# Optimization experiments

Measured on AMD Instinct MI355X. Metric: run time of the kernel, lower is better.

Reference implementation:

```python
import jax, jax.numpy as jnp
import numpy as np

N, C, T, V = 64, 64, 128, 25
OUT, REL = 64, 8
MID = OUT // 2
BN_EPS = 1e-5


def _conv1x1(x, w, b):
    # 1x1 Conv2d: x [n,c,h,w_], w [o,c], b [o]
    return jnp.einsum('nchw,oc->nohw', x, w) + b[None, :, None, None]


def _forward(x, A, w1, b1, w2, b2, w11, b11, w22, b22, w3, b3, w4, b4,
             watt, batt, w5, b5, wc1, bc1, bn_g, bn_b, bn_m, bn_v,
             wc2, bc2, ws, bs, beita, alpha):
    T_ = x.shape[2]
    rel = w1.shape[0]
    x1 = _conv1x1(x, w1, b1)                          # [N,rel,T,V]
    x2 = _conv1x1(x, w2, b2)
    x1_mean, x2_mean = x1.mean(2), x2.mean(2)         # [N,rel,V]
    x1_max, x2_max = x1.max(2), x2.max(2)
    mean_res = x1_mean[:, :, :, None] - x2_mean[:, :, None, :]   # [N,rel,V,V]
    max_res = x1_max[:, :, :, None] - x2_max[:, :, None, :]
    # conv5: grouped 1x1 conv (groups=rel, 2 in-ch/group). The cat(dim=2)+reshape
    # interleaves channels as (mean[c], max[c]) pairs, so per-group it is:
    x_1 = jnp.tanh(w5[None, :, 0, None, None] * mean_res
                   + w5[None, :, 1, None, None] * max_res
                   + b5[None, :, None, None]) * alpha
    x_1 = _conv1x1(x_1, w4, b4)                       # [N,out,V,V]
    x3 = _conv1x1(x, w3, b3)                          # [N,out,T,V]
    x1_res = x_1 + A[None, None]
    # channel-wise spatial correlation attention
    att = jnp.tanh(jnp.einsum('nctu,nctv->ncuv', x1, x2) / T_)
    att = _conv1x1(att, watt, batt)                   # [N,out,V,V]
    global_res = jnp.einsum('nctu,ncuv->nctv', x3, att)
    # Bi_Inter 'channel': global avg pool -> 1x1 -> BN(inference) -> GELU -> 1x1 -> sigmoid
    g = global_res.mean((2, 3), keepdims=True)        # [N,out,1,1]
    h = _conv1x1(g, wc1, bc1)
    h = (h - bn_m[None, :, None, None]) * (bn_g[None, :, None, None]
        / jnp.sqrt(bn_v[None, :, None, None] + BN_EPS)) + bn_b[None, :, None, None]
    h = jax.nn.gelu(h, approximate=False)
    c_att = jax.nn.sigmoid(_conv1x1(h, wc2, bc2))     # [N,out,1,1]
    x1_res = c_att * x1_res
    x1_res = jnp.einsum('ncuv,nctv->nctu', x1_res, x3)  # [N,out,T,V]
    # Bi_Inter 'spatial': mean over T -> 1x1 (out->1) -> sigmoid
    s_att = jax.nn.sigmoid(_conv1x1(x1_res.mean(2, keepdims=True), ws, bs))  # [N,1,1,V]
    global_res = global_res * s_att
    x1_res = x1_res + global_res
    # per-frame spatial correlation (temporal branch)
    x11 = _conv1x1(x, w11, b11)
    x22 = _conv1x1(x, w22, b22)
    xt = jnp.tanh(jnp.einsum('nctv,nctu->ntvu', x11, x22) / rel)  # [N,T,V,V]
    t_res = jnp.einsum('nctu,ntuv->nctv', x3, xt)
    return t_res * beita + x1_res                     # [N,out,T,V]


def setup_inputs() -> dict:
    key = jax.random.key(0)
    ks = jax.random.split(key, 16)
    def nrm(i, shape, s=0.05):
        return jax.random.normal(ks[i], shape, jnp.float32) * s
    return {
        'x': jax.random.normal(ks[0], (N, C, T, V), jnp.float32),
        'A': nrm(1, (V, V), 0.1),
        'w1': nrm(2, (REL, C)), 'b1': jnp.zeros((REL,), jnp.float32),
        'w2': nrm(3, (REL, C)), 'b2': jnp.zeros((REL,), jnp.float32),
        'w11': nrm(4, (REL, C)), 'b11': jnp.zeros((REL,), jnp.float32),
        'w22': nrm(5, (REL, C)), 'b22': jnp.zeros((REL,), jnp.float32),
        'w3': nrm(6, (OUT, C)), 'b3': jnp.zeros((OUT,), jnp.float32),
        'w4': nrm(7, (OUT, REL)), 'b4': jnp.zeros((OUT,), jnp.float32),
        'watt': nrm(8, (OUT, REL)), 'batt': jnp.zeros((OUT,), jnp.float32),
        'w5': nrm(9, (REL, 2)), 'b5': jnp.zeros((REL,), jnp.float32),
        'wc1': nrm(10, (MID, OUT)), 'bc1': jnp.zeros((MID,), jnp.float32),
        'bn_g': jnp.ones((MID,), jnp.float32), 'bn_b': jnp.zeros((MID,), jnp.float32),
        'bn_m': jnp.zeros((MID,), jnp.float32), 'bn_v': jnp.ones((MID,), jnp.float32),
        'wc2': nrm(11, (OUT, MID)), 'bc2': jnp.zeros((OUT,), jnp.float32),
        'ws': nrm(12, (1, OUT)), 'bs': jnp.zeros((1,), jnp.float32),
        'beita': jnp.full((1,), 0.5, jnp.float32),
        'alpha': 1,
    }


def reference(x, A, w1, b1, w2, b2, w11, b11, w22, b22, w3, b3, w4, b4,
              watt, batt, w5, b5, wc1, bc1, bn_g, bn_b, bn_m, bn_v,
              wc2, bc2, ws, bs, beita, alpha):
    return _forward(x, A, w1, b1, w2, b2, w11, b11, w22, b22, w3, b3, w4, b4,
                    watt, batt, w5, b5, wc1, bc1, bn_g, bn_b, bn_m, bn_v,
                    wc2, bc2, ws, bs, beita, alpha)
```

## Files before the change

kernel.cpp:

```cpp
#include <hip/hip_runtime.h>
#include <hip/hip_bf16.h>
#include <math.h>

#define N_   64
#define C_   64
#define T_   128
#define V_   25
#define OUT_ 64
#define REL_ 8
#define MID_ 32
#define TV_  (T_*V_)
#define VV_  (V_*V_)
#define TT2  8

typedef __hip_bfloat16 bf16;
typedef unsigned int uint;
typedef __attribute__((ext_vector_type(8))) short short8v;
typedef __attribute__((ext_vector_type(4))) float float4v;
__device__ __forceinline__ float b2f(bf16 x){ return __bfloat162float(x); }
__device__ __forceinline__ bf16  f2b(float x){ return __float2bfloat16(x); }
__device__ __forceinline__ float bfu(uint u){ return __uint_as_float(u<<16); }
__device__ __forceinline__ float bfh(uint u){ return __uint_as_float(u&0xffff0000u); }
__device__ __forceinline__ float bfs(unsigned short s){ return __uint_as_float(((uint)s)<<16); }

__device__ __forceinline__ float ftanh(float x){
    float cx = fminf(fmaxf(x, -15.f), 15.f);
    float e  = __expf(2.0f*cx);
    return (e - 1.0f) / (e + 1.0f);
}


__global__ __launch_bounds__(256) void k0_prep(
    const float* __restrict__ w1, const float* __restrict__ b1,
    const float* __restrict__ w2, const float* __restrict__ b2,
    const float* __restrict__ w11, const float* __restrict__ b11,
    const float* __restrict__ w22, const float* __restrict__ b22,
    const float* __restrict__ w3, const float* __restrict__ b3,
    unsigned short* __restrict__ WfragUS, float* __restrict__ Bg)
{
    int tid = threadIdx.x;
    for (int idx = tid; idx < 6144; idx += 256){
        int e  = idx & 7;
        int ln = (idx >> 3) & 63;
        int kb = (idx >> 9) & 1;
        int mt = idx >> 10;
        int m = mt*16 + (ln & 15);
        int k = kb*32 + ((ln >> 4) * 8) + e;
        float w;
        if      (m < 8)  w = w1[m*C_+k];
        else if (m < 16) w = w2[(m-8)*C_+k];
        else if (m < 24) w = w11[(m-16)*C_+k];
        else if (m < 32) w = w22[(m-24)*C_+k];
        else             w = w3[(m-32)*C_+k];
        bf16 h = f2b(w);
        WfragUS[idx] = *(unsigned short*)&h;
    }
    if (tid < 96){
        int o = tid; float bb;
        if      (o < 8)  bb = b1[o];
        else if (o < 16) bb = b2[o-8];
        else if (o < 24) bb = b11[o-16];
        else if (o < 32) bb = b22[o-24];
        else             bb = b3[o-32];
        Bg[o] = bb;
    }
}

__global__ __launch_bounds__(256) void k1_mfma(
    const float* __restrict__ x,
    const unsigned short* __restrict__ WfragUS, const float* __restrict__ Bg,
    bf16* __restrict__ x1h, bf16* __restrict__ x2h,
    bf16* __restrict__ x11h, bf16* __restrict__ x22h,
    bf16* __restrict__ x3h)
{
    __shared__ __align__(16) float xl[C_*64];
    __shared__ float Bl[96];
    int bid = blockIdx.x;
    int n = bid / 50, jt = bid % 50;
    int j0 = jt * 64;
    int tid = threadIdx.x;
    for (int e = tid; e < 1024; e += 256){
        int c = e >> 4, j4 = e & 15;
        ((float4*)xl)[e] = ((const float4*)(x + (size_t)(n*C_+c)*TV_ + j0))[j4];
    }
    if (tid < 96) Bl[tid] = Bg[tid];
    __syncthreads();

    int wave = tid >> 6, lane = tid & 63;
    int l15 = lane & 15, lg = lane >> 4;
    const short8v* wf = (const short8v*)WfragUS;
    short8v a[6][2];
    #pragma unroll
    for (int mt = 0; mt < 6; ++mt)
        #pragma unroll
        for (int kb = 0; kb < 2; ++kb)
            a[mt][kb] = wf[(mt*2 + kb)*64 + lane];
    int jw = wave*16 + l15;
    short8v b[2];
    #pragma unroll
    for (int kb = 0; kb < 2; ++kb){
        short8v bb;
        #pragma unroll
        for (int e = 0; e < 8; ++e){
            bf16 h = f2b(xl[(kb*32 + lg*8 + e)*64 + jw]);
            bb[e] = *(short*)&h;
        }
        b[kb] = bb;
    }
    float4v acc[6];
    #pragma unroll
    for (int mt = 0; mt < 6; ++mt) acc[mt] = (float4v){0.f,0.f,0.f,0.f};
    #pragma unroll
    for (int kb = 0; kb < 2; ++kb)
        #pragma unroll
        for (int mt = 0; mt < 6; ++mt)
            acc[mt] = __builtin_amdgcn_mfma_f32_16x16x32_bf16(a[mt][kb], b[kb], acc[mt], 0, 0, 0);

    int pos = j0 + jw;
    #pragma unroll
    for (int mt = 0; mt < 6; ++mt){
        #pragma unroll
        for (int reg = 0; reg < 4; ++reg){
            int o = mt*16 + lg*4 + reg;
            float val = acc[mt][reg] + Bl[o];
            bf16* dst = (o < 8)  ? x1h  + ((size_t)(n*REL_ + o     ))*TV_
                      : (o < 16) ? x2h  + ((size_t)(n*REL_ + o - 8 ))*TV_
                      : (o < 24) ? x11h + ((size_t)(n*REL_ + o - 16))*TV_
                      : (o < 32) ? x22h + ((size_t)(n*REL_ + o - 24))*TV_
                                 : x3h  + ((size_t)(n*OUT_ + o - 32))*TV_;
            dst[pos] = f2b(val);
        }
    }
}

__global__ __launch_bounds__(256) void k_x3bar2(const bf16* __restrict__ x3h,
                                                float* __restrict__ x3bar)
{
    __shared__ __align__(16) float xf[TV_];
    __shared__ float red[V_*8];
    int bid = blockIdx.x;
    int tid = threadIdx.x;
    for (int e = tid; e < 400; e += 256){
        uint4 p = ((const uint4*)(x3h + (size_t)bid*TV_))[e];
        float* d = xf + e*8;
        d[0]=bfu(p.x); d[1]=bfh(p.x); d[2]=bfu(p.y); d[3]=bfh(p.y);
        d[4]=bfu(p.z); d[5]=bfh(p.z); d[6]=bfu(p.w); d[7]=bfh(p.w);
    }
    __syncthreads();
    if (tid < 200){
        int v = tid % V_, g = tid / V_;
        float s = 0.f;
        #pragma unroll
        for (int k=0;k<16;++k) s += xf[(g*16+k)*V_ + v];
        red[g*V_+v] = s;
    }
    __syncthreads();
    if (tid < V_){
        float s = 0.f;
        #pragma unroll
        for (int g=0; g<8; ++g) s += red[g*V_+tid];
        x3bar[(size_t)bid*V_+tid] = s * (1.0f/T_);
    }
}

__global__ __launch_bounds__(256) void k3_mfma(
    const bf16* __restrict__ x1h, const bf16* __restrict__ x2h,
    const float* __restrict__ w5, const float* __restrict__ b5,
    const int* __restrict__ alpha,
    float* __restrict__ att8T, float* __restrict__ xm)
{
    __shared__ __align__(16) unsigned short l1[TV_], l2[TV_];
    __shared__ float mu1l[V_], mu2l[V_], m1l[V_], m2l[V_];
    int bid = blockIdx.x;
    int tid = threadIdx.x;
    int r = bid % REL_;
    for (int e = tid; e < 400; e += 256){
        ((uint4*)l1)[e] = ((const uint4*)(x1h + (size_t)bid*TV_))[e];
        ((uint4*)l2)[e] = ((const uint4*)(x2h + (size_t)bid*TV_))[e];
    }
    __syncthreads();
    if (tid < 50){
        int v = tid % V_;
        const unsigned short* L = (tid < V_) ? l1 : l2;
        float s=0.f, mm=-1e30f;
        for (int t=0;t<T_;++t){
            float a = bfs(L[t*V_+v]);
            s += a; mm = fmaxf(mm, a);
        }
        if (tid < V_){ mu1l[v]=s*(1.0f/T_); m1l[v]=mm; }
        else         { mu2l[v]=s*(1.0f/T_); m2l[v]=mm; }
    }
    __syncthreads();
    int wave = tid >> 6, lane = tid & 63;
    int l15 = lane & 15, lg = lane >> 4;
    int mt = wave >> 1, nt = wave & 1;
    int mu = mt*16 + l15;
    int nv = nt*16 + l15;
    float4v acc = (float4v){0.f,0.f,0.f,0.f};
    #pragma unroll
    for (int kb = 0; kb < 4; ++kb){
        short8v av, bv;
        #pragma unroll
        for (int e = 0; e < 8; ++e){
            int k = kb*32 + lg*8 + e;
            av[e] = (mu < V_) ? (short)l1[k*V_ + mu] : (short)0;
            bv[e] = (nv < V_) ? (short)l2[k*V_ + nv] : (short)0;
        }
        acc = __builtin_amdgcn_mfma_f32_16x16x32_bf16(av, bv, acc, 0, 0, 0);
    }
    #pragma unroll
    for (int reg = 0; reg < 4; ++reg){
        int u = mt*16 + lg*4 + reg;
        if (u < V_ && nv < V_)
            att8T[(size_t)bid*VV_ + nv*V_ + u] = ftanh(acc[reg]*(1.0f/T_));
    }
    float w50=w5[r*2+0], w51=w5[r*2+1], b5r=b5[r];
    float af = (float)alpha[0];
    for (int idx=tid; idx<VV_; idx+=256){
        int u = idx/V_, v = idx%V_;
        float mr = mu1l[u]-mu2l[v];
        float xr = m1l[u]-m2l[v];
        xm[(size_t)bid*VV_+idx] = ftanh(fmaf(w50,mr,fmaf(w51,xr,b5r))) * af;
    }
}

__global__ __launch_bounds__(256) void k68_catt_satt(
    const float* __restrict__ att8T, const float* __restrict__ xm,
    const float* __restrict__ A, const float* __restrict__ x3bar,
    const float* __restrict__ watt, const float* __restrict__ batt,
    const float* __restrict__ wc1, const float* __restrict__ bc1,
    const float* __restrict__ bng, const float* __restrict__ bnb,
    const float* __restrict__ bnm, const float* __restrict__ bnv,
    const float* __restrict__ wc2, const float* __restrict__ bc2,
    const float* __restrict__ w4, const float* __restrict__ b4,
    const float* __restrict__ wsp, const float* __restrict__ bsp,
    float* __restrict__ catt, float* __restrict__ satt)
{
    __shared__ __align__(16) float xml[REL_*VV_];
    __shared__ __align__(16) float xbl[OUT_*V_];
    __shared__ float Al[VV_];
    __shared__ float w4l[OUT_*REL_];
    __shared__ float rs8[REL_*V_];
    __shared__ float gl[OUT_];
    __shared__ float hl[MID_];
    __shared__ float cattl[OUT_];
    __shared__ float scl[OUT_];
    __shared__ float Wl[REL_*V_];
    __shared__ float Yl[V_];
    __shared__ float red[OUT_];
    int n = blockIdx.x, tid = threadIdx.x;
    for (int e=tid; e<1250; e+=256)
        ((float4*)xml)[e] = ((const float4*)(xm + (size_t)n*REL_*VV_))[e];
    for (int e=tid; e<400; e+=256)
        ((float4*)xbl)[e] = ((const float4*)(x3bar + (size_t)n*OUT_*V_))[e];
    for (int e=tid; e<VV_; e+=256) Al[e] = A[e];
    for (int e=tid; e<OUT_*REL_; e+=256) w4l[e] = w4[e];
    if (tid < REL_*V_){
        int r = tid / V_, u = tid % V_;
        const float* p = att8T + (size_t)(n*REL_+r)*VV_;
        float s = 0.f;
        #pragma unroll
        for (int v=0;v<V_;++v) s += p[v*V_ + u];
        rs8[tid] = s;
    }
    __syncthreads();
    if (tid < OUT_){
        int c = tid;
        const float* xb = xbl + c*V_;
        float xbr[V_], sb = 0.f;
        #pragma unroll
        for (int u=0;u<V_;++u){ xbr[u]=xb[u]; sb += xbr[u]; }
        float s = 0.f;
        #pragma unroll
        for (int r=0;r<REL_;++r){
            float d = 0.f;
            #pragma unroll
            for (int u=0;u<V_;++u) d = fmaf(xbr[u], rs8[r*V_+u], d);
            s = fmaf(watt[c*REL_+r], d, s);
        }
        gl[c] = (s + (float)V_*batt[c]*sb) * (1.0f/(float)V_);
    }
    __syncthreads();
    if (tid < MID_){
        float h = bc1[tid];
        for (int c=0;c<OUT_;++c) h = fmaf(wc1[tid*OUT_+c], gl[c], h);
        h = (h - bnm[tid]) * bng[tid] * rsqrtf(bnv[tid] + 1e-5f) + bnb[tid];
        h = 0.5f*h*(1.0f+erff(h*0.70710678118654752f));
        hl[tid]=h;
    }
    __syncthreads();
    if (tid < OUT_){
        float s = bc2[tid];
        for (int m=0;m<MID_;++m) s = fmaf(wc2[tid*MID_+m], hl[m], s);
        float cv = 1.0f/(1.0f+expf(-s));
        cattl[tid] = cv;
        catt[n*OUT_+tid] = cv;
        scl[tid] = wsp[tid]*cv;
    }
    __syncthreads();
    if (tid < REL_*V_){
        int r = tid/V_, v = tid%V_;
        float s = 0.f;
        for (int c=0;c<OUT_;++c) s = fmaf(scl[c]*w4l[c*REL_+r], xbl[c*V_+v], s);
        Wl[tid] = s;
    } else if (tid < REL_*V_ + V_){
        int v = tid - REL_*V_;
        float s = 0.f;
        for (int c=0;c<OUT_;++c) s = fmaf(scl[c], xbl[c*V_+v], s);
        Yl[v] = s;
    }
    __syncthreads();
    if (tid < OUT_){
        float s1 = 0.f;
        #pragma unroll
        for (int v=0;v<V_;++v) s1 += xbl[tid*V_+v];
        red[tid] = scl[tid]*b4[tid]*s1;
    }
    __syncthreads();
    if (tid < V_){
        int u = tid;
        float acc = 0.f;
        #pragma unroll
        for (int r=0;r<REL_;++r){
            const float* xr = xml + r*VV_ + u*V_;
            const float* wr = Wl + r*V_;
            #pragma unroll
            for (int v=0;v<V_;++v) acc = fmaf(xr[v], wr[v], acc);
        }
        #pragma unroll
        for (int v=0;v<V_;++v) acc = fmaf(Al[u*V_+v], Yl[v], acc);
        float beta = 0.f;
        for (int c=0;c<OUT_;++c) beta += red[c];
        satt[n*V_+u] = 1.0f/(1.0f+expf(-(bsp[0]+acc+beta)));
    }
}

__global__ __launch_bounds__(256) void k_comb4(
    const bf16* __restrict__ x3h,
    const float* __restrict__ att8T, const float* __restrict__ xm,
    const float* __restrict__ A,
    const float* __restrict__ watt, const float* __restrict__ batt,
    const float* __restrict__ w4, const float* __restrict__ b4,
    const float* __restrict__ catt, const float* __restrict__ satt,
    bf16* __restrict__ combh)
{
    __shared__ __align__(16) unsigned short x3s[TV_];
    __shared__ float Ml[VV_];
    __shared__ float sl[V_];
    __shared__ __align__(16) unsigned short cst[TV_];
    int bid = blockIdx.x;
    int n = bid >> 6, c = bid & 63;
    int tid = threadIdx.x;
    for (int e = tid; e < 400; e += 256)
        ((uint4*)x3s)[e] = ((const uint4*)(x3h + (size_t)bid*TV_))[e];
    if (tid < V_) sl[tid] = satt[n*V_+tid];
    float ca = catt[bid];
    float w4r[REL_], war[REL_];
    #pragma unroll
    for (int r=0;r<REL_;++r){ w4r[r] = w4[c*REL_+r]; war[r] = watt[c*REL_+r]; }
    float b4c = b4[c], bac = batt[c];
    const float* xmn = xm    + (size_t)n*REL_*VV_;
    const float* a8n = att8T + (size_t)n*REL_*VV_;
    __syncthreads();
    for (int e = tid; e < VV_; e += 256){
        int w = e/V_;
        float xv = b4c, av = bac;
        #pragma unroll
        for (int r=0;r<REL_;++r){
            xv = fmaf(w4r[r], xmn[r*VV_ + e], xv);
            av = fmaf(war[r], a8n[r*VV_ + e], av);
        }
        Ml[e] = ca*(xv + A[e]) + av*sl[w];
    }
    __syncthreads();
    int wave = tid >> 6, lane = tid & 63;
    int l15 = lane & 15, lg = lane >> 4;
    short8v bfr[2];
    #pragma unroll
    for (int nt = 0; nt < 2; ++nt){
        int w = nt*16 + l15;
        short8v bv;
        #pragma unroll
        for (int e = 0; e < 8; ++e){
            int u = lg*8 + e;
            float mv = (w < V_ && u < V_) ? Ml[w*V_ + u] : 0.f;
            bf16 h = f2b(mv);
            bv[e] = *(short*)&h;
        }
        bfr[nt] = bv;
    }
    #pragma unroll
    for (int mi = 0; mi < 2; ++mi){
        int mt = wave*2 + mi;
        int t = mt*16 + l15;
        short8v av;
        #pragma unroll
        for (int e = 0; e < 8; ++e){
            int u = lg*8 + e;
            av[e] = (u < V_) ? (short)x3s[t*V_ + u] : (short)0;
        }
        #pragma unroll
        for (int nt = 0; nt < 2; ++nt){
            float4v acc = (float4v){0.f,0.f,0.f,0.f};
            acc = __builtin_amdgcn_mfma_f32_16x16x32_bf16(av, bfr[nt], acc, 0, 0, 0);
            int w = nt*16 + l15;
            if (w < V_){
                #pragma unroll
                for (int reg = 0; reg < 4; ++reg){
                    int tr = mt*16 + lg*4 + reg;
                    bf16 h = f2b(acc[reg]);
                    cst[tr*V_ + w] = *(unsigned short*)&h;
                }
            }
        }
    }
    __syncthreads();
    for (int e = tid; e < 400; e += 256)
        ((uint4*)(combh + (size_t)bid*TV_))[e] = ((const uint4*)cst)[e];
}

__global__ __launch_bounds__(512) void k9_xt(
    const bf16* __restrict__ x11h, const bf16* __restrict__ x22h,
    bf16* __restrict__ xtg)
{
    __shared__ __align__(16) float l11[REL_*TT2*V_];
    __shared__ __align__(16) float l22[REL_*TT2*V_];
    int bid = blockIdx.x;
    int n = bid >> 4, tt = bid & 15;
    int t0 = tt * TT2;
    int tid = threadIdx.x;
    for (int e = tid; e < 400; e += 512){
        int half = (e >= 200);
        int i = half ? e-200 : e;
        int r = i / 25, ch = i % 25;
        const bf16* src = (half ? x22h : x11h) + (size_t)(n*REL_+r)*TV_ + t0*V_ + ch*8;
        uint4 p = *(const uint4*)src;
        float* d = (half ? l22 : l11) + i*8;
        d[0]=bfu(p.x); d[1]=bfh(p.x); d[2]=bfu(p.y); d[3]=bfh(p.y);
        d[4]=bfu(p.z); d[5]=bfh(p.z); d[6]=bfu(p.w); d[7]=bfh(p.w);
    }
    __syncthreads();
    for (int idx = tid; idx < TT2*1024; idx += 512){
        int ti  = idx >> 10;
        int rem = idx & 1023;
        int lane = (rem >> 3) & 63;
        int e = rem & 7;
        int u = ((lane >> 4) << 3) + e;
        int v = ((rem >> 9) << 4) + (lane & 15);
        float val = 0.f;
        if (u < V_ && v < V_){
            float s = 0.f;
            #pragma unroll
            for (int r = 0; r < REL_; ++r)
                s = fmaf(l11[r*200 + ti*V_ + u], l22[r*200 + ti*V_ + v], s);
            val = ftanh(s * 0.125f);
        }
        xtg[(size_t)(n*T_ + t0 + ti)*1024 + rem] = f2b(val);
    }
}

__global__ __launch_bounds__(512) void k10_mfma(
    const bf16* __restrict__ xtg,
    const bf16* __restrict__ x3h, const bf16* __restrict__ combh,
    const float* __restrict__ beita, float* __restrict__ out)
{
    __shared__ __align__(16) char stg[25600];
    int bid = blockIdx.x;
    int n = bid >> 5, rem = bid & 31;
    int tt = rem >> 1, ch = rem & 1;
    int t0 = tt * TT2, c0 = ch * 32;
    int tid = threadIdx.x;
    for (int e = tid; e < 1600; e += 512){
        int cl = e / 50, w = e % 50;
        size_t base = (size_t)(n*OUT_ + c0 + cl)*TV_ + (size_t)t0*V_;
        uint4 p = (w < 25) ? ((const uint4*)(combh + base))[w]
                           : ((const uint4*)(x3h  + base))[w-25];
        *(uint4*)(stg + cl*800 + (w<25 ? w*16 : 400 + (w-25)*16)) = p;
    }
    __syncthreads();
    float bt = beita[0];
    int wave = tid >> 6, lane = tid & 63;
    int ti = wave;
    int t = t0 + ti;
    int l15 = lane & 15, lg = lane >> 4;
    const short8v* bp = (const short8v*)(xtg + (size_t)(n*T_ + t)*1024);
    short8v bfr[2];
    bfr[0] = bp[lane];
    bfr[1] = bp[64 + lane];
    short8v afr[2];
    #pragma unroll
    for (int mt = 0; mt < 2; ++mt){
        short8v av;
        #pragma unroll
        for (int e = 0; e < 8; ++e){
            int u = lg*8 + e;
            int cl = mt*16 + l15;
            av[e] = (u < V_) ? *(const short*)(stg + cl*800 + 400 + ti*50 + u*2)
                             : (short)0;
        }
        afr[mt] = av;
    }
    float4v acc[2][2];
    #pragma unroll
    for (int mt = 0; mt < 2; ++mt)
        #pragma unroll
        for (int nt = 0; nt < 2; ++nt){
            acc[mt][nt] = (float4v){0.f,0.f,0.f,0.f};
            acc[mt][nt] = __builtin_amdgcn_mfma_f32_16x16x32_bf16(
                              afr[mt], bfr[nt], acc[mt][nt], 0, 0, 0);
        }
    #pragma unroll
    for (int mt = 0; mt < 2; ++mt){
        #pragma unroll
        for (int nt = 0; nt < 2; ++nt){
            int v = nt*16 + l15;
            if (v >= V_) continue;
            #pragma unroll
            for (int r = 0; r < 4; ++r){
                int cl = mt*16 + lg*4 + r;
                float cmb = bfs(*(const unsigned short*)(stg + cl*800 + ti*50 + v*2));
                float val = fmaf(bt, acc[mt][nt][r], cmb);
                out[(size_t)(n*OUT_ + c0 + cl)*TV_ + (size_t)t*V_ + v] = val;
            }
        }
    }
}

extern "C" void kernel_launch(void* const* d_in, const int* in_sizes, int n_in,
                              void* d_out, int out_size, void* d_ws, size_t ws_size,
                              hipStream_t stream)
{
    const float* x    = (const float*)d_in[0];
    const float* A    = (const float*)d_in[1];
    const float* w1   = (const float*)d_in[2];  const float* b1  = (const float*)d_in[3];
    const float* w2   = (const float*)d_in[4];  const float* b2  = (const float*)d_in[5];
    const float* w11  = (const float*)d_in[6];  const float* b11 = (const float*)d_in[7];
    const float* w22  = (const float*)d_in[8];  const float* b22 = (const float*)d_in[9];
    const float* w3   = (const float*)d_in[10]; const float* b3  = (const float*)d_in[11];
    const float* w4   = (const float*)d_in[12]; const float* b4  = (const float*)d_in[13];
    const float* watt = (const float*)d_in[14]; const float* batt= (const float*)d_in[15];
    const float* w5   = (const float*)d_in[16]; const float* b5  = (const float*)d_in[17];
    const float* wc1  = (const float*)d_in[18]; const float* bc1 = (const float*)d_in[19];
    const float* bng  = (const float*)d_in[20]; const float* bnb = (const float*)d_in[21];
    const float* bnm  = (const float*)d_in[22]; const float* bnv = (const float*)d_in[23];
    const float* wc2  = (const float*)d_in[24]; const float* bc2 = (const float*)d_in[25];
    const float* wsp  = (const float*)d_in[26]; const float* bsp = (const float*)d_in[27];
    const float* beita= (const float*)d_in[28];
    const int*  alpha = (const int*)d_in[29];
    float* out = (float*)d_out;

    char* wsb = (char*)d_ws;
    size_t off = 0;
    auto alloc = [&](size_t bytes)->char*{
        char* p = wsb + off;
        off += (bytes + 255) & ~(size_t)255;
        return p;
    };
    bf16*  x1h   = (bf16*) alloc((size_t)N_*REL_*TV_*2);
    bf16*  x2h   = (bf16*) alloc((size_t)N_*REL_*TV_*2);
    bf16*  x11h  = (bf16*) alloc((size_t)N_*REL_*TV_*2);
    bf16*  x22h  = (bf16*) alloc((size_t)N_*REL_*TV_*2);
    bf16*  x3h   = (bf16*) alloc((size_t)N_*OUT_*TV_*2);
    bf16*  combh = (bf16*) alloc((size_t)N_*OUT_*TV_*2);
    bf16*  xtg   = (bf16*) alloc((size_t)N_*T_*1024*2);
    float* att8T = (float*)alloc((size_t)N_*REL_*VV_*4);
    float* xm    = (float*)alloc((size_t)N_*REL_*VV_*4);
    float* x3bar = (float*)alloc((size_t)N_*OUT_*V_*4);
    float* catt  = (float*)alloc((size_t)N_*OUT_*4);
    float* satt  = (float*)alloc((size_t)N_*V_*4);
    unsigned short* WfragUS = (unsigned short*)alloc((size_t)6144*2);
    float* Bg    = (float*)alloc((size_t)96*4);
    (void)ws_size; (void)n_in; (void)in_sizes; (void)out_size;

    k0_prep<<<1, 256, 0, stream>>>(w1,b1, w2,b2, w11,b11, w22,b22, w3,b3, WfragUS, Bg);
    k1_mfma<<<N_*50, 256, 0, stream>>>(x, WfragUS, Bg, x1h, x2h, x11h, x22h, x3h);
    k_x3bar2<<<N_*OUT_, 256, 0, stream>>>(x3h, x3bar);
    k3_mfma<<<N_*REL_, 256, 0, stream>>>(x1h, x2h, w5, b5, alpha, att8T, xm);
    k9_xt<<<N_*16, 512, 0, stream>>>(x11h, x22h, xtg);
    k68_catt_satt<<<N_, 256, 0, stream>>>(att8T, xm, A, x3bar, watt, batt,
                                          wc1, bc1, bng, bnb, bnm, bnv, wc2, bc2,
                                          w4, b4, wsp, bsp, catt, satt);
    k_comb4<<<N_*OUT_, 256, 0, stream>>>(x3h, att8T, xm, A, watt, batt, w4, b4,
                                         catt, satt, combh);
    k10_mfma<<<N_*32, 512, 0, stream>>>(xtg, x3h, combh, beita, out);
}
```

Before: 113.7 us.

## Compute x3 time-mean from input via linearity and merge k3/k9 into one launch

Drops the separate x3bar kernel, which re-read all of x3 from memory. Each k1 block now atomically accumulates per-(n,c,v) sums of the raw input tile into a new buffer, and x3bar is rebuilt as w3·mean(x)+b3 using the linearity of the 1x1 conv. The k3 and k9 kernels, plus the new x3bar step, are merged into one launch that branches on block index, saving launches and letting the independent stages run together. In exchange it adds a memset, global float atomics (non-deterministic summation order), and a heterogeneous grid that uses 512 threads where the old k3 used 256.

New measurement: 119.0 us. 4.6% more time.

```diff
diff --git a/kernel.cpp b/kernel.cpp
--- a/kernel.cpp
+++ b/kernel.cpp
@@ -71,7 +71,7 @@
     const unsigned short* __restrict__ WfragUS, const float* __restrict__ Bg,
     bf16* __restrict__ x1h, bf16* __restrict__ x2h,
     bf16* __restrict__ x11h, bf16* __restrict__ x22h,
-    bf16* __restrict__ x3h)
+    bf16* __restrict__ x3h, float* __restrict__ xbarg)
 {
     __shared__ __align__(16) float xl[C_*64];
     __shared__ float Bl[96];
@@ -131,96 +131,138 @@
             dst[pos] = f2b(val);
         }
     }
-}
-
-__global__ __launch_bounds__(256) void k_x3bar2(const bf16* __restrict__ x3h,
-                                                float* __restrict__ x3bar)
-{
-    __shared__ __align__(16) float xf[TV_];
-    __shared__ float red[V_*8];
-    int bid = blockIdx.x;
-    int tid = threadIdx.x;
-    for (int e = tid; e < 400; e += 256){
-        uint4 p = ((const uint4*)(x3h + (size_t)bid*TV_))[e];
-        float* d = xf + e*8;
-        d[0]=bfu(p.x); d[1]=bfh(p.x); d[2]=bfu(p.y); d[3]=bfh(p.y);
-        d[4]=bfu(p.z); d[5]=bfh(p.z); d[6]=bfu(p.w); d[7]=bfh(p.w);
-    }
-    __syncthreads();
-    if (tid < 200){
-        int v = tid % V_, g = tid / V_;
+    int jm = j0 % 25;
+    for (int idx = tid; idx < 1600; idx += 256){
+        int c = idx / 25, v = idx - c*25;
+        int j = v - jm; if (j < 0) j += 25;
         float s = 0.f;
         #pragma unroll
-        for (int k=0;k<16;++k) s += xf[(g*16+k)*V_ + v];
-        red[g*V_+v] = s;
-    }
-    __syncthreads();
-    if (tid < V_){
-        float s = 0.f;
-        #pragma unroll
-        for (int g=0; g<8; ++g) s += red[g*V_+tid];
-        x3bar[(size_t)bid*V_+tid] = s * (1.0f/T_);
-    }
-}
-
-__global__ __launch_bounds__(256) void k3_mfma(
+        for (int q = 0; q < 3; ++q){
+            if (j < 64){ s += xl[c*64 + j]; j += 25; }
+        }
+        atomicAdd(&xbarg[((size_t)n*C_ + c)*V_ + v], s);
+    }
+}
+
+__global__ __launch_bounds__(512) void k39(
     const bf16* __restrict__ x1h, const bf16* __restrict__ x2h,
     const float* __restrict__ w5, const float* __restrict__ b5,
     const int* __restrict__ alpha,
-    float* __restrict__ att8T, float* __restrict__ xm)
-{
-    __shared__ __align__(16) unsigned short l1[TV_], l2[TV_];
-    __shared__ float mu1l[V_], mu2l[V_], m1l[V_], m2l[V_];
+    float* __restrict__ att8T, float* __restrict__ xm,
+    const bf16* __restrict__ x11h, const bf16* __restrict__ x22h,
+    bf16* __restrict__ xtg,
+    const float* __restrict__ xbarg, const float* __restrict__ w3,
+    const float* __restrict__ b3, float* __restrict__ x3bar)
+{
+    __shared__ __align__(16) char ubuf[13216];
     int bid = blockIdx.x;
     int tid = threadIdx.x;
-    int r = bid % REL_;
-    for (int e = tid; e < 400; e += 256){
-        ((uint4*)l1)[e] = ((const uint4*)(x1h + (size_t)bid*TV_))[e];
-        ((uint4*)l2)[e] = ((const uint4*)(x2h + (size_t)bid*TV_))[e];
-    }
-    __syncthreads();
-    if (tid < 50){
-        int v = tid % V_;
-        const unsigned short* L = (tid < V_) ? l1 : l2;
-        float s=0.f, mm=-1e30f;
-        for (int t=0;t<T_;++t){
-            float a = bfs(L[t*V_+v]);
-            s += a; mm = fmaxf(mm, a);
-        }
-        if (tid < V_){ mu1l[v]=s*(1.0f/T_); m1l[v]=mm; }
-        else         { mu2l[v]=s*(1.0f/T_); m2l[v]=mm; }
-    }
-    __syncthreads();
-    int wave = tid >> 6, lane = tid & 63;
-    int l15 = lane & 15, lg = lane >> 4;
-    int mt = wave >> 1, nt = wave & 1;
-    int mu = mt*16 + l15;
-    int nv = nt*16 + l15;
-    float4v acc = (float4v){0.f,0.f,0.f,0.f};
-    #pragma unroll
-    for (int kb = 0; kb < 4; ++kb){
-        short8v av, bv;
-        #pragma unroll
-        for (int e = 0; e < 8; ++e){
-            int k = kb*32 + lg*8 + e;
-            av[e] = (mu < V_) ? (short)l1[k*V_ + mu] : (short)0;
-            bv[e] = (nv < V_) ? (short)l2[k*V_ + nv] : (short)0;
-        }
-        acc = __builtin_amdgcn_mfma_f32_16x16x32_bf16(av, bv, acc, 0, 0, 0);
-    }
-    #pragma unroll
-    for (int reg = 0; reg < 4; ++reg){
-        int u = mt*16 + lg*4 + reg;
-        if (u < V_ && nv < V_)
-            att8T[(size_t)bid*VV_ + nv*V_ + u] = ftanh(acc[reg]*(1.0f/T_));
-    }
-    float w50=w5[r*2+0], w51=w5[r*2+1], b5r=b5[r];
-    float af = (float)alpha[0];
-    for (int idx=tid; idx<VV_; idx+=256){
-        int u = idx/V_, v = idx%V_;
-        float mr = mu1l[u]-mu2l[v];
-        float xr = m1l[u]-m2l[v];
-        xm[(size_t)bid*VV_+idx] = ftanh(fmaf(w50,mr,fmaf(w51,xr,b5r))) * af;
+    if (bid < 512){
+        unsigned short* l1 = (unsigned short*)ubuf;
+        unsigned short* l2 = (unsigned short*)(ubuf + 6400);
+        float* mu1l = (float*)(ubuf + 12800);
+        float* mu2l = (float*)(ubuf + 12800 + 104);
+        float* m1l  = (float*)(ubuf + 12800 + 208);
+        float* m2l  = (float*)(ubuf + 12800 + 312);
+        int r = bid % REL_;
+        for (int e = tid; e < 400; e += 512){
+            ((uint4*)l1)[e] = ((const uint4*)(x1h + (size_t)bid*TV_))[e];
+            ((uint4*)l2)[e] = ((const uint4*)(x2h + (size_t)bid*TV_))[e];
+        }
+        __syncthreads();
+        if (tid < 50){
+            int v = tid % V_;
+            const unsigned short* L = (tid < V_) ? l1 : l2;
+            float s=0.f, mm=-1e30f;
+            for (int t=0;t<T_;++t){
+                float a = bfs(L[t*V_+v]);
+                s += a; mm = fmaxf(mm, a);
+            }
+            if (tid < V_){ mu1l[v]=s*(1.0f/T_); m1l[v]=mm; }
+            else         { mu2l[v]=s*(1.0f/T_); m2l[v]=mm; }
+        }
+        __syncthreads();
+        int wave = tid >> 6, lane = tid & 63;
+        if (wave < 4){
+            int l15 = lane & 15, lg = lane >> 4;
+            int mt = wave >> 1, nt = wave & 1;
+            int mu = mt*16 + l15;
+            int nv = nt*16 + l15;
+            float4v acc = (float4v){0.f,0.f,0.f,0.f};
+            #pragma unroll
+            for (int kb = 0; kb < 4; ++kb){
+                short8v av, bv;
+                #pragma unroll
+                for (int e = 0; e < 8; ++e){
+                    int k = kb*32 + lg*8 + e;
+                    av[e] = (mu < V_) ? (short)l1[k*V_ + mu] : (short)0;
+                    bv[e] = (nv < V_) ? (short)l2[k*V_ + nv] : (short)0;
+                }
+                acc = __builtin_amdgcn_mfma_f32_16x16x32_bf16(av, bv, acc, 0, 0, 0);
+            }
+            #pragma unroll
+            for (int reg = 0; reg < 4; ++reg){
+                int u = mt*16 + lg*4 + reg;
+                if (u < V_ && nv < V_)
+                    att8T[(size_t)bid*VV_ + nv*V_ + u] = ftanh(acc[reg]*(1.0f/T_));
+            }
+        }
+        float w50=w5[r*2+0], w51=w5[r*2+1], b5r=b5[r];
+        float af = (float)alpha[0];
+        for (int idx=tid; idx<VV_; idx+=512){
+            int u = idx/V_, v = idx%V_;
+            float mr = mu1l[u]-mu2l[v];
+            float xr = m1l[u]-m2l[v];
+            xm[(size_t)bid*VV_+idx] = ftanh(fmaf(w50,mr,fmaf(w51,xr,b5r))) * af;
+        }
+    } else if (bid < 1536){
+        int b9 = bid - 512;
+        int n = b9 >> 4, tt = b9 & 15;
+        int t0 = tt * TT2;
+        float* l11 = (float*)ubuf;
+        float* l22 = (float*)(ubuf + 6400);
+        for (int e = tid; e < 400; e += 512){
+            int half = (e >= 200);
+            int i = half ? e-200 : e;
+            int r = i / 25, ch = i % 25;
+            const bf16* src = (half ? x22h : x11h) + (size_t)(n*REL_+r)*TV_ + t0*V_ + ch*8;
+            uint4 p = *(const uint4*)src;
+            float* d = (half ? l22 : l11) + i*8;
+            d[0]=bfu(p.x); d[1]=bfh(p.x); d[2]=bfu(p.y); d[3]=bfh(p.y);
+            d[4]=bfu(p.z); d[5]=bfh(p.z); d[6]=bfu(p.w); d[7]=bfh(p.w);
+        }
+        __syncthreads();
+        for (int idx = tid; idx < TT2*1024; idx += 512){
+            int ti  = idx >> 10;
+            int rem = idx & 1023;
+            int lane = (rem >> 3) & 63;
+            int e = rem & 7;
+            int u = ((lane >> 4) << 3) + e;
+            int v = ((rem >> 9) << 4) + (lane & 15);
+            float val = 0.f;
+            if (u < V_ && v < V_){
+                float s = 0.f;
+                #pragma unroll
+                for (int r = 0; r < REL_; ++r)
+                    s = fmaf(l11[r*200 + ti*V_ + u], l22[r*200 + ti*V_ + v], s);
+                val = ftanh(s * 0.125f);
+            }
+            xtg[(size_t)(n*T_ + t0 + ti)*1024 + rem] = f2b(val);
+        }
+    } else {
+        int n = bid - 1536;
+        float* xbm = (float*)ubuf;
+        for (int e = tid; e < 1600; e += 512)
+            xbm[e] = xbarg[(size_t)n*1600 + e] * (1.0f/(float)T_);
+        __syncthreads();
+        for (int idx = tid; idx < 1600; idx += 512){
+            int c = idx / 25, v = idx - c*25;
+            float s = b3[c];
+            #pragma unroll
+            for (int k = 0; k < C_; ++k)
+                s = fmaf(w3[c*C_ + k], xbm[k*25 + v], s);
+            x3bar[(size_t)n*1600 + idx] = s;
+        }
     }
 }
 
@@ -243,7 +285,6 @@
     __shared__ float rs8[REL_*V_];
     __shared__ float gl[OUT_];
     __shared__ float hl[MID_];
-    __shared__ float cattl[OUT_];
     __shared__ float scl[OUT_];
     __shared__ float Wl[REL_*V_];
     __shared__ float Yl[V_];
@@ -293,7 +334,6 @@
         float s = bc2[tid];
         for (int m=0;m<MID_;++m) s = fmaf(wc2[tid*MID_+m], hl[m], s);
         float cv = 1.0f/(1.0f+expf(-s));
-        cattl[tid] = cv;
         catt[n*OUT_+tid] = cv;
         scl[tid] = wsp[tid]*cv;
     }
@@ -417,46 +457,6 @@
     __syncthreads();
     for (int e = tid; e < 400; e += 256)
         ((uint4*)(combh + (size_t)bid*TV_))[e] = ((const uint4*)cst)[e];
-}
-
-__global__ __launch_bounds__(512) void k9_xt(
-    const bf16* __restrict__ x11h, const bf16* __restrict__ x22h,
-    bf16* __restrict__ xtg)
-{
-    __shared__ __align__(16) float l11[REL_*TT2*V_];
-    __shared__ __align__(16) float l22[REL_*TT2*V_];
-    int bid = blockIdx.x;
-    int n = bid >> 4, tt = bid & 15;
-    int t0 = tt * TT2;
-    int tid = threadIdx.x;
-    for (int e = tid; e < 400; e += 512){
-        int half = (e >= 200);
-        int i = half ? e-200 : e;
-        int r = i / 25, ch = i % 25;
-        const bf16* src = (half ? x22h : x11h) + (size_t)(n*REL_+r)*TV_ + t0*V_ + ch*8;
-        uint4 p = *(const uint4*)src;
-        float* d = (half ? l22 : l11) + i*8;
-        d[0]=bfu(p.x); d[1]=bfh(p.x); d[2]=bfu(p.y); d[3]=bfh(p.y);
-        d[4]=bfu(p.z); d[5]=bfh(p.z); d[6]=bfu(p.w); d[7]=bfh(p.w);
-    }
-    __syncthreads();
-    for (int idx = tid; idx < TT2*1024; idx += 512){
-        int ti  = idx >> 10;
-        int rem = idx & 1023;
-        int lane = (rem >> 3) & 63;
-        int e = rem & 7;
-        int u = ((lane >> 4) << 3) + e;
-        int v = ((rem >> 9) << 4) + (lane & 15);
-        float val = 0.f;
-        if (u < V_ && v < V_){
-            float s = 0.f;
-            #pragma unroll
-            for (int r = 0; r < REL_; ++r)
-                s = fmaf(l11[r*200 + ti*V_ + u], l22[r*200 + ti*V_ + v], s);
-            val = ftanh(s * 0.125f);
-        }
-        xtg[(size_t)(n*T_ + t0 + ti)*1024 + rem] = f2b(val);
-    }
 }
 
 __global__ __launch_bounds__(512) void k10_mfma(
@@ -566,17 +566,18 @@
     float* att8T = (float*)alloc((size_t)N_*REL_*VV_*4);
     float* xm    = (float*)alloc((size_t)N_*REL_*VV_*4);
     float* x3bar = (float*)alloc((size_t)N_*OUT_*V_*4);
+    float* xbarg = (float*)alloc((size_t)N_*C_*V_*4);
     float* catt  = (float*)alloc((size_t)N_*OUT_*4);
     float* satt  = (float*)alloc((size_t)N_*V_*4);
     unsigned short* WfragUS = (unsigned short*)alloc((size_t)6144*2);
     float* Bg    = (float*)alloc((size_t)96*4);
     (void)ws_size; (void)n_in; (void)in_sizes; (void)out_size;
 
+    hipMemsetAsync(xbarg, 0, (size_t)N_*C_*V_*4, stream);
     k0_prep<<<1, 256, 0, stream>>>(w1,b1, w2,b2, w11,b11, w22,b22, w3,b3, WfragUS, Bg);
-    k1_mfma<<<N_*50, 256, 0, stream>>>(x, WfragUS, Bg, x1h, x2h, x11h, x22h, x3h);
-    k_x3bar2<<<N_*OUT_, 256, 0, stream>>>(x3h, x3bar);
-    k3_mfma<<<N_*REL_, 256, 0, stream>>>(x1h, x2h, w5, b5, alpha, att8T, xm);
-    k9_xt<<<N_*16, 512, 0, stream>>>(x11h, x22h, xtg);
+    k1_mfma<<<N_*50, 256, 0, stream>>>(x, WfragUS, Bg, x1h, x2h, x11h, x22h, x3h, xbarg);
+    k39<<<1600, 512, 0, stream>>>(x1h, x2h, w5, b5, alpha, att8T, xm,
+                                  x11h, x22h, xtg, xbarg, w3, b3, x3bar);
     k68_catt_satt<<<N_, 256, 0, stream>>>(att8T, xm, A, x3bar, watt, batt,
                                           wc1, bc1, bng, bnb, bnm, bnv, wc2, bc2,
                                           w4, b4, wsp, bsp, catt, satt);
```
